# Kernel tuning notes

Hardware: AMD Instinct MI355X
Metric: run time of the kernel (lower is better)

The kernel has to match this reference:

```python
import jax, jax.numpy as jnp
import numpy as np

N = 50000      # total nodes in batch
E = 640000     # directed edges
G = 64         # graphs in batch
F_IN = 24      # node features
H = 128        # hidden dim
L = 4          # num GCN layers
BN_EPS = 1e-5


def setup_inputs() -> dict:
    key = jax.random.key(0)
    ks = jax.random.split(key, 12)
    s = 0.05  # weight init scale
    return {
        "x": jax.random.normal(ks[0], (N, F_IN), jnp.float32),
        "edge_index": jax.random.randint(ks[1], (2, E), 0, N, dtype=jnp.int32),
        "batch": jnp.sort(jax.random.randint(ks[2], (N,), 0, G, dtype=jnp.int32)),
        "W0": jax.random.normal(ks[3], (F_IN, H), jnp.float32) * s,
        "Wh": jax.random.normal(ks[4], (L - 1, H, H), jnp.float32) * s,
        "b": jnp.zeros((L, H), jnp.float32),
        "bn_gamma": jnp.ones((L, H), jnp.float32),
        "bn_beta": jnp.zeros((L, H), jnp.float32),
        "bn_mean": jax.random.normal(ks[5], (L, H), jnp.float32) * 0.01,
        "bn_var": jnp.ones((L, H), jnp.float32),
        "pool_W": jax.random.normal(ks[6], (2 * H, H), jnp.float32) * s,
        "pool_b": jnp.zeros((H,), jnp.float32),
        "out_W": jax.random.normal(ks[7], (H, H // 2), jnp.float32) * s,
        "out_b": jnp.zeros((H // 2,), jnp.float32),
    }


def reference(x, edge_index, batch, W0, Wh, b, bn_gamma, bn_beta, bn_mean,
              bn_var, pool_W, pool_b, out_W, out_b):
    n = x.shape[0]
    loop = jnp.arange(n, dtype=edge_index.dtype)
    src = jnp.concatenate([edge_index[0], loop])  # [E+N] with self-loops
    dst = jnp.concatenate([edge_index[1], loop])
    # symmetric GCN normalization: deg includes self-loops, so deg >= 1
    deg = jax.ops.segment_sum(jnp.ones_like(dst, x.dtype), dst, num_segments=n)
    dis = jax.lax.rsqrt(deg)
    coef = (dis[src] * dis[dst])[:, None]  # [E+N, 1]

    def gcn_conv(h, W, bias):
        h = h @ W                                   # [N, H]
        msg = h[src] * coef                         # gather + scale
        return jax.ops.segment_sum(msg, dst, num_segments=n) + bias

    Ws = [W0] + [Wh[i] for i in range(Wh.shape[0])]
    h = x
    for i in range(L):
        h = gcn_conv(h, Ws[i], b[i])
        # BatchNorm1d (eval mode) + ReLU; dropout = identity in eval
        h = (h - bn_mean[i]) * jax.lax.rsqrt(bn_var[i] + BN_EPS) * bn_gamma[i] + bn_beta[i]
        h = jax.nn.relu(h)

    counts = jax.ops.segment_sum(jnp.ones((n,), h.dtype), batch, num_segments=G)
    x_mean = jax.ops.segment_sum(h, batch, num_segments=G) / jnp.maximum(counts, 1.0)[:, None]
    x_max = jax.ops.segment_max(h, batch, num_segments=G)
    x_pooled = jnp.concatenate([x_mean, x_max], axis=1)        # [G, 2H]
    x_pooled = jax.nn.relu(x_pooled @ pool_W + pool_b)         # global_pool MLP
    return x_pooled @ out_W + out_b                            # embedding head [G, H//2]
```

## Files before the change

kernel.cpp:

```cpp
#include <hip/hip_runtime.h>
#include <hip/hip_bf16.h>
#include <hip/hip_fp16.h>

#define HD 128
#define BN_EPS 1e-5f

typedef __attribute__((ext_vector_type(8))) short short8;
typedef __attribute__((ext_vector_type(8))) _Float16 half8;
typedef __attribute__((ext_vector_type(4))) float f32x4;

__device__ inline unsigned short f2bf(float v, float& rem) {
    unsigned u = __float_as_uint(v);
    unsigned r = (u + 0x7FFFu + ((u >> 16) & 1u)) >> 16;
    rem = v - __uint_as_float(r << 16);
    return (unsigned short)r;
}

__global__ void k_count(const int* __restrict__ dst, int* __restrict__ counts,
                        unsigned short* __restrict__ ord, int E) {
    int i = blockIdx.x * blockDim.x + threadIdx.x;
    for (; i < E; i += gridDim.x * blockDim.x) {
        int pos = atomicAdd(&counts[dst[i]], 1);
        ord[i] = (unsigned short)pos;
    }
}

__global__ void k_scan1(const int* __restrict__ counts, int* __restrict__ offs,
                        int* __restrict__ bsums, int n) {
    __shared__ int s[256];
    int t = threadIdx.x, i = blockIdx.x * 256 + t;
    int v = (i < n) ? counts[i] : 0;
    s[t] = v; __syncthreads();
    for (int d = 1; d < 256; d <<= 1) {
        int x = (t >= d) ? s[t - d] : 0;
        __syncthreads(); s[t] += x; __syncthreads();
    }
    if (i < n) offs[i] = s[t] - v;
    if (t == 255) bsums[blockIdx.x] = s[255];
}

__global__ void k_scan2(int* __restrict__ bsums, int nb,
                        const int* __restrict__ batch, int* __restrict__ starts,
                        int n, int G) {
    __shared__ int s[256];
    int t = threadIdx.x;
    int v = (t < nb) ? bsums[t] : 0;
    s[t] = v; __syncthreads();
    for (int d = 1; d < 256; d <<= 1) {
        int x = (t >= d) ? s[t - d] : 0;
        __syncthreads(); s[t] += x; __syncthreads();
    }
    if (t < nb) bsums[t] = s[t] - v;
    if (t <= G) {
        int lo = 0, hi = n;
        while (lo < hi) {
            int mid = (lo + hi) >> 1;
            if (batch[mid] < t) lo = mid + 1; else hi = mid;
        }
        starts[t] = lo;
    }
}

__global__ void k_scan3(int* __restrict__ offs, const int* __restrict__ bsums,
                        const int* __restrict__ counts, float* __restrict__ dis, int n) {
    int i = blockIdx.x * 256 + threadIdx.x;
    if (i < n) {
        offs[i] += bsums[blockIdx.x];
        dis[i] = rsqrtf((float)(counts[i] + 1));
    }
}

__global__ void k_fill(const int* __restrict__ src, const int* __restrict__ dst,
                       const unsigned short* __restrict__ ord, const int* __restrict__ offs,
                       unsigned short* __restrict__ esrc, int E) {
    int i = blockIdx.x * blockDim.x + threadIdx.x;
    for (; i < E; i += gridDim.x * blockDim.x) {
        int s = src[i], d = dst[i];
        esrc[offs[d] + ord[i]] = (unsigned short)s;
    }
}

__global__ void k_wsplit(const float* __restrict__ W0, const float* __restrict__ Wh,
                         unsigned short* __restrict__ whi0, unsigned short* __restrict__ wlo0,
                         unsigned short* __restrict__ whf, unsigned short* __restrict__ wlf) {
    int idx = blockIdx.x * 256 + threadIdx.x;
    int l = idx >> 14, rest = idx & 16383;
    int k = rest >> 7, c = rest & 127;
    int cb = c >> 4, kc = k >> 5;
    int lane = (c & 15) | (((k & 31) >> 3) << 4);
    int j = k & 7;
    if (l == 0) {
        if (k >= 32) return;
        float val = (k < 24) ? W0[k * HD + c] : 0.f;
        float rem, rem2;
        unsigned short hi = f2bf(val, rem);
        unsigned short lo = f2bf(rem, rem2);
        size_t addr = (size_t)(cb * 64 + lane) * 8 + j;
        whi0[addr] = hi; wlo0[addr] = lo;
    } else {
        float val = Wh[(size_t)(l - 1) * HD * HD + (size_t)k * HD + c];
        __half h = __float2half(val);
        float rem = val - __half2float(h);
        __half lo = __float2half(rem);
        size_t addr = (size_t)(l - 1) * 16384 + (size_t)((cb * 4 + kc) * 64 + lane) * 8 + j;
        whf[addr] = __half_as_ushort(h);
        wlf[addr] = __half_as_ushort(lo);
    }
}

__global__ void k_agg_x(const float* __restrict__ in, const int* __restrict__ offs,
                        const int* __restrict__ counts, const unsigned short* __restrict__ esrc,
                        const float* __restrict__ dis, unsigned short* __restrict__ ohi,
                        unsigned short* __restrict__ olo, int n) {
    const int FQ = 6, GRP = 8;
    int grp = threadIdx.x / GRP;
    int lane = threadIdx.x % GRP;
    int node = blockIdx.x * (blockDim.x / GRP) + grp;
    if (node >= n) return;
    int rowblk = node >> 4, rr = node & 15;

    if (lane == FQ) {
        size_t base = (size_t)rowblk * 512 + (size_t)(rr + 48) * 8;
        ushort4 z = make_ushort4(0, 0, 0, 0);
        *(ushort4*)(ohi + base) = z; *(ushort4*)(ohi + base + 4) = z;
        *(ushort4*)(olo + base) = z; *(ushort4*)(olo + base + 4) = z;
    }
    if (lane >= FQ) return;

    const float4* in4 = reinterpret_cast<const float4*>(in);
    float dn = dis[node];
    float sl = dn * dn;
    float4 a = in4[(size_t)node * FQ + lane];
    float4 accA = make_float4(sl * a.x, sl * a.y, sl * a.z, sl * a.w);
    float4 accB = make_float4(0.f, 0.f, 0.f, 0.f);

    int e = offs[node], end = e + counts[node];
    for (; e + 3 < end; e += 4) {
        int s0 = esrc[e],     s1 = esrc[e + 1];
        int s2 = esrc[e + 2], s3 = esrc[e + 3];
        float c0 = dis[s0] * dn, c1 = dis[s1] * dn;
        float c2 = dis[s2] * dn, c3 = dis[s3] * dn;
        float4 v0 = in4[(size_t)s0 * FQ + lane];
        float4 v1 = in4[(size_t)s1 * FQ + lane];
        float4 v2 = in4[(size_t)s2 * FQ + lane];
        float4 v3 = in4[(size_t)s3 * FQ + lane];
        accA.x = fmaf(c0, v0.x, fmaf(c2, v2.x, accA.x));
        accA.y = fmaf(c0, v0.y, fmaf(c2, v2.y, accA.y));
        accA.z = fmaf(c0, v0.z, fmaf(c2, v2.z, accA.z));
        accA.w = fmaf(c0, v0.w, fmaf(c2, v2.w, accA.w));
        accB.x = fmaf(c1, v1.x, fmaf(c3, v3.x, accB.x));
        accB.y = fmaf(c1, v1.y, fmaf(c3, v3.y, accB.y));
        accB.z = fmaf(c1, v1.z, fmaf(c3, v3.z, accB.z));
        accB.w = fmaf(c1, v1.w, fmaf(c3, v3.w, accB.w));
    }
    for (; e < end; ++e) {
        int s0 = esrc[e];
        float c0 = dis[s0] * dn;
        float4 v0 = in4[(size_t)s0 * FQ + lane];
        accA.x = fmaf(c0, v0.x, accA.x);
        accA.y = fmaf(c0, v0.y, accA.y);
        accA.z = fmaf(c0, v0.z, accA.z);
        accA.w = fmaf(c0, v0.w, accA.w);
    }
    float4 acc = make_float4(accA.x + accB.x, accA.y + accB.y,
                             accA.z + accB.z, accA.w + accB.w);

    int f0 = lane * 4;
    int lidx = rr | (((f0 & 31) >> 3) << 4);
    int j0 = f0 & 7;
    size_t base = (size_t)rowblk * 512 + (size_t)lidx * 8 + j0;
    float r0, r1, r2, r3, d0;
    ushort4 hi, lo;
    hi.x = f2bf(acc.x, r0); hi.y = f2bf(acc.y, r1);
    hi.z = f2bf(acc.z, r2); hi.w = f2bf(acc.w, r3);
    lo.x = f2bf(r0, d0); lo.y = f2bf(r1, d0);
    lo.z = f2bf(r2, d0); lo.w = f2bf(r3, d0);
    *(ushort4*)(ohi + base) = hi;
    *(ushort4*)(olo + base) = lo;
}

__global__ void k_agg_h(const __half* __restrict__ in, const int* __restrict__ offs,
                        const int* __restrict__ counts, const unsigned short* __restrict__ esrc,
                        const float* __restrict__ dis, unsigned short* __restrict__ af, int n) {
    int grp = threadIdx.x >> 5;
    int lane = threadIdx.x & 31;
    int node = blockIdx.x * 8 + grp;
    if (node >= n) return;
    int rowblk = node >> 4, rr = node & 15;

    const float2* in8 = reinterpret_cast<const float2*>(in);
    float dn = dis[node];
    float sl = dn * dn;

    float2 raw = in8[(size_t)node * 32 + lane];
    __half2 p0 = *(__half2*)&raw.x, p1 = *(__half2*)&raw.y;
    float2 f0v = __half22float2(p0), f1v = __half22float2(p1);
    float4 accA = make_float4(sl * f0v.x, sl * f0v.y, sl * f1v.x, sl * f1v.y);
    float4 accB = make_float4(0.f, 0.f, 0.f, 0.f);

    int e = offs[node], end = e + counts[node];
    for (; e + 3 < end; e += 4) {
        int s0 = esrc[e],     s1 = esrc[e + 1];
        int s2 = esrc[e + 2], s3 = esrc[e + 3];
        float c0 = dis[s0] * dn, c1 = dis[s1] * dn;
        float c2 = dis[s2] * dn, c3 = dis[s3] * dn;
        float2 w0 = in8[(size_t)s0 * 32 + lane];
        float2 w1 = in8[(size_t)s1 * 32 + lane];
        float2 w2 = in8[(size_t)s2 * 32 + lane];
        float2 w3 = in8[(size_t)s3 * 32 + lane];
        float2 a0 = __half22float2(*(__half2*)&w0.x), b0 = __half22float2(*(__half2*)&w0.y);
        float2 a1 = __half22float2(*(__half2*)&w1.x), b1 = __half22float2(*(__half2*)&w1.y);
        float2 a2 = __half22float2(*(__half2*)&w2.x), b2 = __half22float2(*(__half2*)&w2.y);
        float2 a3 = __half22float2(*(__half2*)&w3.x), b3 = __half22float2(*(__half2*)&w3.y);
        accA.x = fmaf(c0, a0.x, fmaf(c2, a2.x, accA.x));
        accA.y = fmaf(c0, a0.y, fmaf(c2, a2.y, accA.y));
        accA.z = fmaf(c0, b0.x, fmaf(c2, b2.x, accA.z));
        accA.w = fmaf(c0, b0.y, fmaf(c2, b2.y, accA.w));
        accB.x = fmaf(c1, a1.x, fmaf(c3, a3.x, accB.x));
        accB.y = fmaf(c1, a1.y, fmaf(c3, a3.y, accB.y));
        accB.z = fmaf(c1, b1.x, fmaf(c3, b3.x, accB.z));
        accB.w = fmaf(c1, b1.y, fmaf(c3, b3.y, accB.w));
    }
    for (; e < end; ++e) {
        int s0 = esrc[e];
        float c0 = dis[s0] * dn;
        float2 w0 = in8[(size_t)s0 * 32 + lane];
        float2 a0 = __half22float2(*(__half2*)&w0.x), b0 = __half22float2(*(__half2*)&w0.y);
        accA.x = fmaf(c0, a0.x, accA.x);
        accA.y = fmaf(c0, a0.y, accA.y);
        accA.z = fmaf(c0, b0.x, accA.z);
        accA.w = fmaf(c0, b0.y, accA.w);
    }
    float4 acc = make_float4(accA.x + accB.x, accA.y + accB.y,
                             accA.z + accB.z, accA.w + accB.w);

    int f0 = lane * 4;
    int kc = f0 >> 5;
    int lidx = rr | (((f0 & 31) >> 3) << 4);
    int j0 = f0 & 7;
    size_t base = ((size_t)rowblk * 4 + kc) * 512 + (size_t)lidx * 8 + j0;
    ushort4 hv;
    hv.x = __half_as_ushort(__float2half(acc.x));
    hv.y = __half_as_ushort(__float2half(acc.y));
    hv.z = __half_as_ushort(__float2half(acc.z));
    hv.w = __half_as_ushort(__float2half(acc.w));
    *(ushort4*)(af + base) = hv;
}

__global__ __launch_bounds__(256) void k_gemm_m(
        const unsigned short* __restrict__ agh, const unsigned short* __restrict__ agl,
        const unsigned short* __restrict__ wh, const unsigned short* __restrict__ wl,
        const float* __restrict__ bias, const float* __restrict__ gamma,
        const float* __restrict__ beta, const float* __restrict__ mean,
        const float* __restrict__ var, __half* __restrict__ outh, int n) {
    __shared__ unsigned short lbh[8 * 512];
    __shared__ unsigned short lbl[8 * 512];
    int tid = threadIdx.x;
    for (int i = tid; i < 1024; i += 256) {
        ((ushort4*)lbh)[i] = ((const ushort4*)wh)[i];
        ((ushort4*)lbl)[i] = ((const ushort4*)wl)[i];
    }
    __syncthreads();

    int wave = tid >> 6, lane = tid & 63;
    int grb0 = blockIdx.x * 8 + wave * 2;

    f32x4 acc[2][8] = {};

    short8 a0h = *(const short8*)(agh + (size_t)grb0 * 512 + lane * 8);
    short8 a0l = *(const short8*)(agl + (size_t)grb0 * 512 + lane * 8);
    short8 a1h = *(const short8*)(agh + (size_t)(grb0 + 1) * 512 + lane * 8);
    short8 a1l = *(const short8*)(agl + (size_t)(grb0 + 1) * 512 + lane * 8);
    #pragma unroll
    for (int cb = 0; cb < 8; ++cb) {
        short8 bh = *(const short8*)(lbh + (size_t)(cb * 64 + lane) * 8);
        short8 bl = *(const short8*)(lbl + (size_t)(cb * 64 + lane) * 8);
        acc[0][cb] = __builtin_amdgcn_mfma_f32_16x16x32_bf16(a0h, bh, acc[0][cb], 0, 0, 0);
        acc[0][cb] = __builtin_amdgcn_mfma_f32_16x16x32_bf16(a0h, bl, acc[0][cb], 0, 0, 0);
        acc[0][cb] = __builtin_amdgcn_mfma_f32_16x16x32_bf16(a0l, bh, acc[0][cb], 0, 0, 0);
        acc[1][cb] = __builtin_amdgcn_mfma_f32_16x16x32_bf16(a1h, bh, acc[1][cb], 0, 0, 0);
        acc[1][cb] = __builtin_amdgcn_mfma_f32_16x16x32_bf16(a1h, bl, acc[1][cb], 0, 0, 0);
        acc[1][cb] = __builtin_amdgcn_mfma_f32_16x16x32_bf16(a1l, bh, acc[1][cb], 0, 0, 0);
    }

    int colbase = lane & 15;
    float scv[8], shv[8];
    #pragma unroll
    for (int cb = 0; cb < 8; ++cb) {
        int c = cb * 16 + colbase;
        float s = gamma[c] * rsqrtf(var[c] + BN_EPS);
        scv[cb] = s;
        shv[cb] = beta[c] + (bias[c] - mean[c]) * s;
    }
    int r0 = (lane >> 4) * 4;
    #pragma unroll
    for (int rb = 0; rb < 2; ++rb) {
        int rowb = (grb0 + rb) * 16 + r0;
        #pragma unroll
        for (int rg = 0; rg < 4; ++rg) {
            int row = rowb + rg;
            if (row < n) {
                #pragma unroll
                for (int cb = 0; cb < 8; ++cb) {
                    float v = fmaxf(fmaf(acc[rb][cb][rg], scv[cb], shv[cb]), 0.f);
                    outh[(size_t)row * HD + cb * 16 + colbase] = __float2half(v);
                }
            }
        }
    }
}

template<bool POOL>
__global__ __launch_bounds__(256) void k_gemm_h(
        const unsigned short* __restrict__ af,
        const unsigned short* __restrict__ wh, const unsigned short* __restrict__ wl,
        const float* __restrict__ bias, const float* __restrict__ gamma,
        const float* __restrict__ beta, const float* __restrict__ mean,
        const float* __restrict__ var, __half* __restrict__ outh,
        const int* __restrict__ batch, float* __restrict__ gsum,
        unsigned int* __restrict__ gmax, int n) {
    __shared__ unsigned short lbh[16384];
    __shared__ unsigned short lbl[16384];
    int tid = threadIdx.x;
    for (int i = tid; i < 4096; i += 256) {
        ((ushort4*)lbh)[i] = ((const ushort4*)wh)[i];
        ((ushort4*)lbl)[i] = ((const ushort4*)wl)[i];
    }
    __syncthreads();

    int wave = tid >> 6, lane = tid & 63;
    int grb0 = blockIdx.x * 8 + wave * 2;

    f32x4 acc[2][8] = {};

    #pragma unroll
    for (int kc = 0; kc < 4; ++kc) {
        half8 a0 = *(const half8*)(af + ((size_t)grb0 * 4 + kc) * 512 + lane * 8);
        half8 a1 = *(const half8*)(af + ((size_t)(grb0 + 1) * 4 + kc) * 512 + lane * 8);
        #pragma unroll
        for (int cb = 0; cb < 8; ++cb) {
            half8 bh = *(const half8*)(lbh + (size_t)((cb * 4 + kc) * 64 + lane) * 8);
            half8 bl = *(const half8*)(lbl + (size_t)((cb * 4 + kc) * 64 + lane) * 8);
            acc[0][cb] = __builtin_amdgcn_mfma_f32_16x16x32_f16(a0, bh, acc[0][cb], 0, 0, 0);
            acc[0][cb] = __builtin_amdgcn_mfma_f32_16x16x32_f16(a0, bl, acc[0][cb], 0, 0, 0);
            acc[1][cb] = __builtin_amdgcn_mfma_f32_16x16x32_f16(a1, bh, acc[1][cb], 0, 0, 0);
            acc[1][cb] = __builtin_amdgcn_mfma_f32_16x16x32_f16(a1, bl, acc[1][cb], 0, 0, 0);
        }
    }

    int colbase = lane & 15;
    float scv[8], shv[8];
    #pragma unroll
    for (int cb = 0; cb < 8; ++cb) {
        int c = cb * 16 + colbase;
        float s = gamma[c] * rsqrtf(var[c] + BN_EPS);
        scv[cb] = s;
        shv[cb] = beta[c] + (bias[c] - mean[c]) * s;
    }
    int r0 = (lane >> 4) * 4;

    if (!POOL) {
        #pragma unroll
        for (int rb = 0; rb < 2; ++rb) {
            int rowb = (grb0 + rb) * 16 + r0;
            #pragma unroll
            for (int rg = 0; rg < 4; ++rg) {
                int row = rowb + rg;
                if (row < n) {
                    #pragma unroll
                    for (int cb = 0; cb < 8; ++cb) {
                        float v = fmaxf(fmaf(acc[rb][cb][rg], scv[cb], shv[cb]), 0.f);
                        outh[(size_t)row * HD + cb * 16 + colbase] = __float2half(v);
                    }
                }
            }
        }
    } else {
        int row0 = blockIdx.x * 128;
        int row_hi = min(n - 1, row0 + 127);
        int g_lo = batch[row0];
        int g_hi = batch[row_hi];

        int gval[2][4];
        #pragma unroll
        for (int rb = 0; rb < 2; ++rb) {
            int rowb = (grb0 + rb) * 16 + r0;
            #pragma unroll
            for (int rg = 0; rg < 4; ++rg) {
                int row = rowb + rg;
                gval[rb][rg] = (row < n) ? batch[row] : -1;
            }
        }

        __syncthreads();
        float* lds_sum = reinterpret_cast<float*>(lbh);
        unsigned int* lds_max = reinterpret_cast<unsigned int*>(lbh) + 512;

        for (int gbase = g_lo; gbase <= g_hi; gbase += 4) {
            for (int i = tid; i < 512; i += 256) {
                lds_sum[i] = 0.f;
                lds_max[i] = 0u;
            }
            __syncthreads();
            #pragma unroll
            for (int rb = 0; rb < 2; ++rb) {
                #pragma unroll
                for (int rg = 0; rg < 4; ++rg) {
                    int g = gval[rb][rg];
                    if (g >= gbase && g < gbase + 4) {
                        int sbase = (g - gbase) * 128;
                        #pragma unroll
                        for (int cb = 0; cb < 8; ++cb) {
                            float v = fmaxf(fmaf(acc[rb][cb][rg], scv[cb], shv[cb]), 0.f);
                            int col = cb * 16 + colbase;
                            atomicAdd(&lds_sum[sbase + col], v);
                            atomicMax(&lds_max[sbase + col], __float_as_uint(v));
                        }
                    }
                }
            }
            __syncthreads();
            for (int i = tid; i < 512; i += 256) {
                int s = i >> 7, col = i & 127;
                int g = gbase + s;
                if (g <= g_hi) {
                    atomicAdd(&gsum[g * HD + col], lds_sum[i]);
                    atomicMax(&gmax[g * HD + col], lds_max[i]);
                }
            }
            __syncthreads();
        }
    }
}

__global__ void k_head(const float* __restrict__ gsum, const unsigned int* __restrict__ gmax,
                       const int* __restrict__ starts, const float* __restrict__ pool_W,
                       const float* __restrict__ pool_b, const float* __restrict__ out_W,
                       const float* __restrict__ out_b, float* __restrict__ out) {
    int g = blockIdx.x, t = threadIdx.x;
    __shared__ float pooled[2 * HD];
    __shared__ float hid_s[HD];
    float cntf = fmaxf((float)(starts[g + 1] - starts[g]), 1.f);
    pooled[t] = gsum[g * HD + t] / cntf;
    pooled[HD + t] = __uint_as_float(gmax[g * HD + t]);
    __syncthreads();
    float acc = pool_b[t];
    for (int k = 0; k < 2 * HD; ++k)
        acc += pooled[k] * pool_W[k * HD + t];
    hid_s[t] = fmaxf(acc, 0.f);
    __syncthreads();
    if (t < 64) {
        float a2 = out_b[t];
        for (int j = 0; j < HD; ++j)
            a2 += hid_s[j] * out_W[j * 64 + t];
        out[g * 64 + t] = a2;
    }
}

extern "C" void kernel_launch(void* const* d_in, const int* in_sizes, int n_in,
                              void* d_out, int out_size, void* d_ws, size_t ws_size,
                              hipStream_t stream) {
    const float* x        = (const float*)d_in[0];
    const int*   eidx     = (const int*)d_in[1];
    const int*   batch    = (const int*)d_in[2];
    const float* W0       = (const float*)d_in[3];
    const float* Wh       = (const float*)d_in[4];
    const float* b        = (const float*)d_in[5];
    const float* bn_gamma = (const float*)d_in[6];
    const float* bn_beta  = (const float*)d_in[7];
    const float* bn_mean  = (const float*)d_in[8];
    const float* bn_var   = (const float*)d_in[9];
    const float* pool_W   = (const float*)d_in[10];
    const float* pool_b   = (const float*)d_in[11];
    const float* out_W    = (const float*)d_in[12];
    const float* out_b    = (const float*)d_in[13];
    float* out = (float*)d_out;

    const int N = in_sizes[2];
    const int E = in_sizes[1] / 2;
    const int L = in_sizes[5] / HD;
    const int G = out_size / (HD / 2);

    const int* src = eidx;
    const int* dst = eidx + E;

    const int NBLK = (N + 127) / 128;
    const size_t NRB = (size_t)NBLK * 8;

    char* p = (char*)d_ws;
    __half* hf   = (__half*)p; p += (size_t)NBLK * 128 * HD * 2;
    unsigned short* af  = (unsigned short*)p; p += NRB * 4 * 512 * 2;
    unsigned short* agh = (unsigned short*)p; p += NRB * 512 * 2;
    unsigned short* agl = (unsigned short*)p; p += NRB * 512 * 2;
    unsigned short* whi0 = (unsigned short*)p; p += (size_t)16384 * 2;
    unsigned short* wlo0 = (unsigned short*)p; p += (size_t)16384 * 2;
    unsigned short* whf  = (unsigned short*)p; p += (size_t)3 * 16384 * 2;
    unsigned short* wlf  = (unsigned short*)p; p += (size_t)3 * 16384 * 2;
    unsigned short* esrc = (unsigned short*)p; p += (((size_t)E * 2 + 15) & ~15ull);
    unsigned short* ord  = (unsigned short*)p; p += (((size_t)E * 2 + 15) & ~15ull);
    int*   counts  = (int*)p;   p += (size_t)N * 4;
    float* dis     = (float*)p; p += (size_t)N * 4;
    int*   offs    = (int*)p;   p += (size_t)(N + 1) * 4;
    int*   bsums   = (int*)p;   p += 256 * 4;
    float* gsum    = (float*)p; p += (size_t)G * HD * 4;
    unsigned int* gmax = (unsigned int*)p; p += (size_t)G * HD * 4;
    int*   starts  = (int*)p;   p += (size_t)(G + 1) * 4;
    (void)ws_size; (void)n_in;

    hipMemsetAsync(counts, 0, (size_t)N * 4, stream);
    hipMemsetAsync(gsum, 0, (size_t)G * HD * 8, stream);

    const int NB = (N + 255) / 256;

    k_count<<<1024, 256, 0, stream>>>(dst, counts, ord, E);
    k_scan1<<<NB, 256, 0, stream>>>(counts, offs, bsums, N);
    k_scan2<<<1, 256, 0, stream>>>(bsums, NB, batch, starts, N, G);
    k_scan3<<<NB, 256, 0, stream>>>(offs, bsums, counts, dis, N);
    k_fill<<<1024, 256, 0, stream>>>(src, dst, ord, offs, esrc, E);
    k_wsplit<<<256, 256, 0, stream>>>(W0, Wh, whi0, wlo0, whf, wlf);

    k_agg_x<<<(N + 31) / 32, 256, 0, stream>>>(x, offs, counts, esrc, dis, agh, agl, N);
    k_gemm_m<<<NBLK, 256, 0, stream>>>(agh, agl, whi0, wlo0, b, bn_gamma, bn_beta,
                                       bn_mean, bn_var, hf, N);

    for (int l = 1; l < L; ++l) {
        k_agg_h<<<(N + 7) / 8, 256, 0, stream>>>(hf, offs, counts, esrc, dis, af, N);
        const unsigned short* wh_l = whf + (size_t)(l - 1) * 16384;
        const unsigned short* wl_l = wlf + (size_t)(l - 1) * 16384;
        if (l < L - 1)
            k_gemm_h<false><<<NBLK, 256, 0, stream>>>(af, wh_l, wl_l,
                b + l * HD, bn_gamma + l * HD, bn_beta + l * HD,
                bn_mean + l * HD, bn_var + l * HD, hf, batch, gsum, gmax, N);
        else
            k_gemm_h<true><<<NBLK, 256, 0, stream>>>(af, wh_l, wl_l,
                b + l * HD, bn_gamma + l * HD, bn_beta + l * HD,
                bn_mean + l * HD, bn_var + l * HD, nullptr, batch, gsum, gmax, N);
    }

    k_head<<<G, HD, 0, stream>>>(gsum, gmax, starts, pool_W, pool_b, out_W, out_b, out);
}
```

Measured before the change: 275.0 us.

## Split aggregation by feature column groups and replace LDS pooling atomics with shuffles

The hidden-layer aggregation kernel now assigns each node's 128 features across four column-group blocks, with 8 lanes per node and 32 nodes per block. The block index is interleaved so each 32-column slice is handled by separate blocks, aiming for better cache locality on gathered rows and more parallelism per edge. The pooling epilogue of the last GEMM drops the LDS-staged atomic sum/max and its barriers. It instead reduces per graph in registers with wave shuffles and issues global atomics directly, at the cost of looping over every graph in the block's range.

New measurement: 267.8 us. 1.03x faster.

```diff
diff --git a/kernel.cpp b/kernel.cpp
--- a/kernel.cpp
+++ b/kernel.cpp
@@ -182,19 +182,23 @@
 __global__ void k_agg_h(const __half* __restrict__ in, const int* __restrict__ offs,
                         const int* __restrict__ counts, const unsigned short* __restrict__ esrc,
                         const float* __restrict__ dis, unsigned short* __restrict__ af, int n) {
-    int grp = threadIdx.x >> 5;
-    int lane = threadIdx.x & 31;
-    int node = blockIdx.x * 8 + grp;
+    int b = blockIdx.x;
+    int cg = (b & 7) >> 1;
+    int chunk = ((b >> 3) << 1) | (b & 1);
+    int grp = threadIdx.x >> 3;
+    int lane = threadIdx.x & 7;
+    int node = chunk * 32 + grp;
     if (node >= n) return;
     int rowblk = node >> 4, rr = node & 15;
+    int fq = cg * 8 + lane;
 
     const float2* in8 = reinterpret_cast<const float2*>(in);
     float dn = dis[node];
     float sl = dn * dn;
 
-    float2 raw = in8[(size_t)node * 32 + lane];
-    __half2 p0 = *(__half2*)&raw.x, p1 = *(__half2*)&raw.y;
-    float2 f0v = __half22float2(p0), f1v = __half22float2(p1);
+    float2 raw = in8[(size_t)node * 32 + fq];
+    float2 f0v = __half22float2(*(__half2*)&raw.x);
+    float2 f1v = __half22float2(*(__half2*)&raw.y);
     float4 accA = make_float4(sl * f0v.x, sl * f0v.y, sl * f1v.x, sl * f1v.y);
     float4 accB = make_float4(0.f, 0.f, 0.f, 0.f);
 
@@ -204,10 +208,10 @@
         int s2 = esrc[e + 2], s3 = esrc[e + 3];
         float c0 = dis[s0] * dn, c1 = dis[s1] * dn;
         float c2 = dis[s2] * dn, c3 = dis[s3] * dn;
-        float2 w0 = in8[(size_t)s0 * 32 + lane];
-        float2 w1 = in8[(size_t)s1 * 32 + lane];
-        float2 w2 = in8[(size_t)s2 * 32 + lane];
-        float2 w3 = in8[(size_t)s3 * 32 + lane];
+        float2 w0 = in8[(size_t)s0 * 32 + fq];
+        float2 w1 = in8[(size_t)s1 * 32 + fq];
+        float2 w2 = in8[(size_t)s2 * 32 + fq];
+        float2 w3 = in8[(size_t)s3 * 32 + fq];
         float2 a0 = __half22float2(*(__half2*)&w0.x), b0 = __half22float2(*(__half2*)&w0.y);
         float2 a1 = __half22float2(*(__half2*)&w1.x), b1 = __half22float2(*(__half2*)&w1.y);
         float2 a2 = __half22float2(*(__half2*)&w2.x), b2 = __half22float2(*(__half2*)&w2.y);
@@ -224,7 +228,7 @@
     for (; e < end; ++e) {
         int s0 = esrc[e];
         float c0 = dis[s0] * dn;
-        float2 w0 = in8[(size_t)s0 * 32 + lane];
+        float2 w0 = in8[(size_t)s0 * 32 + fq];
         float2 a0 = __half22float2(*(__half2*)&w0.x), b0 = __half22float2(*(__half2*)&w0.y);
         accA.x = fmaf(c0, a0.x, accA.x);
         accA.y = fmaf(c0, a0.y, accA.y);
@@ -234,11 +238,9 @@
     float4 acc = make_float4(accA.x + accB.x, accA.y + accB.y,
                              accA.z + accB.z, accA.w + accB.w);
 
-    int f0 = lane * 4;
-    int kc = f0 >> 5;
-    int lidx = rr | (((f0 & 31) >> 3) << 4);
-    int j0 = f0 & 7;
-    size_t base = ((size_t)rowblk * 4 + kc) * 512 + (size_t)lidx * 8 + j0;
+    int lidx = rr | ((lane >> 1) << 4);
+    int j0 = (lane & 1) * 4;
+    size_t base = ((size_t)rowblk * 4 + cg) * 512 + (size_t)lidx * 8 + j0;
     ushort4 hv;
     hv.x = __half_as_ushort(__float2half(acc.x));
     hv.y = __half_as_ushort(__float2half(acc.y));
@@ -392,43 +394,30 @@
             }
         }
 
-        __syncthreads();
-        float* lds_sum = reinterpret_cast<float*>(lbh);
-        unsigned int* lds_max = reinterpret_cast<unsigned int*>(lbh) + 512;
-
-        for (int gbase = g_lo; gbase <= g_hi; gbase += 4) {
-            for (int i = tid; i < 512; i += 256) {
-                lds_sum[i] = 0.f;
-                lds_max[i] = 0u;
-            }
-            __syncthreads();
+        for (int g = g_lo; g <= g_hi; ++g) {
             #pragma unroll
-            for (int rb = 0; rb < 2; ++rb) {
+            for (int cb = 0; cb < 8; ++cb) {
+                float s = 0.f, m = 0.f;
                 #pragma unroll
-                for (int rg = 0; rg < 4; ++rg) {
-                    int g = gval[rb][rg];
-                    if (g >= gbase && g < gbase + 4) {
-                        int sbase = (g - gbase) * 128;
-                        #pragma unroll
-                        for (int cb = 0; cb < 8; ++cb) {
+                for (int rb = 0; rb < 2; ++rb) {
+                    #pragma unroll
+                    for (int rg = 0; rg < 4; ++rg) {
+                        if (gval[rb][rg] == g) {
                             float v = fmaxf(fmaf(acc[rb][cb][rg], scv[cb], shv[cb]), 0.f);
-                            int col = cb * 16 + colbase;
-                            atomicAdd(&lds_sum[sbase + col], v);
-                            atomicMax(&lds_max[sbase + col], __float_as_uint(v));
+                            s += v;
+                            m = fmaxf(m, v);
                         }
                     }
                 }
-            }
-            __syncthreads();
-            for (int i = tid; i < 512; i += 256) {
-                int s = i >> 7, col = i & 127;
-                int g = gbase + s;
-                if (g <= g_hi) {
-                    atomicAdd(&gsum[g * HD + col], lds_sum[i]);
-                    atomicMax(&gmax[g * HD + col], lds_max[i]);
+                s += __shfl_xor(s, 16);
+                m = fmaxf(m, __shfl_xor(m, 16));
+                s += __shfl_xor(s, 32);
+                m = fmaxf(m, __shfl_xor(m, 32));
+                if (lane < 16 && (s != 0.f || m != 0.f)) {
+                    atomicAdd(&gsum[g * HD + cb * 16 + colbase], s);
+                    atomicMax(&gmax[g * HD + cb * 16 + colbase], __float_as_uint(m));
                 }
             }
-            __syncthreads();
         }
     }
 }
@@ -523,8 +512,10 @@
     k_gemm_m<<<NBLK, 256, 0, stream>>>(agh, agl, whi0, wlo0, b, bn_gamma, bn_beta,
                                        bn_mean, bn_var, hf, N);
 
+    const int CHUNKS = (N + 31) / 32;
+    const int AGG_GRID = 8 * ((CHUNKS + 1) / 2);
     for (int l = 1; l < L; ++l) {
-        k_agg_h<<<(N + 7) / 8, 256, 0, stream>>>(hf, offs, counts, esrc, dis, af, N);
+        k_agg_h<<<AGG_GRID, 256, 0, stream>>>(hf, offs, counts, esrc, dis, af, N);
         const unsigned short* wh_l = whf + (size_t)(l - 1) * 16384;
         const unsigned short* wl_l = wlf + (size_t)(l - 1) * 16384;
         if (l < L - 1)
```
